# Kernel optimization log

Hardware: AMD Instinct MI355X
Metric: run time of the kernel (lower is better)

Reference implementation:

```python
import jax, jax.numpy as jnp
import numpy as np

VOCAB = 96
HIDDEN = 128
DEPTH = 500          # total ReLU iterations per character (num_layers=1)
BPTT_DEPTH = 20      # only affects backward (truncated BPTT)
EPS = 1e-6


def _rms_norm(x, scale):
    # x: (B, H). RMSNorm: x / sqrt(mean(x^2) + eps) * scale
    rms = jnp.sqrt(jnp.mean(x * x, axis=-1, keepdims=True) + EPS)
    return x / rms * scale


def setup_inputs() -> dict:
    key = jax.random.key(0)
    ks = jax.random.split(key, 6)
    B, S = 64, 32
    chars = jax.random.randint(ks[0], (B, S), 0, VOCAB)
    hidden = jnp.zeros((B, HIDDEN), dtype=jnp.float32)
    # embedding ~ N(0, 0.02)
    embed_w = 0.02 * jax.random.normal(ks[1], (VOCAB, HIDDEN), dtype=jnp.float32)
    # orthogonal recurrent weight, scaled by 1/sqrt(num_layers)=1 (num_layers=1)
    W = jnp.linalg.qr(jax.random.normal(ks[2], (HIDDEN, HIDDEN), dtype=jnp.float32))[0]
    b = jnp.zeros((HIDDEN,), dtype=jnp.float32)
    pre_scale = jnp.ones((HIDDEN,), dtype=jnp.float32)
    post_scale = jnp.ones((HIDDEN,), dtype=jnp.float32)
    # readout: xavier-uniform (VOCAB, HIDDEN), zero bias
    limit = float(np.sqrt(6.0 / (VOCAB + HIDDEN)))
    readout_w = jax.random.uniform(ks[3], (VOCAB, HIDDEN), dtype=jnp.float32,
                                   minval=-limit, maxval=limit)
    readout_b = jnp.zeros((VOCAB,), dtype=jnp.float32)
    return {"chars": chars, "hidden": hidden, "embed_w": embed_w, "W": W,
            "b": b, "pre_scale": pre_scale, "post_scale": post_scale,
            "readout_w": readout_w, "readout_b": readout_b}


def reference(chars, hidden, embed_w, W, b, pre_scale, post_scale,
              readout_w, readout_b):
    # chars: (B, S) int; hidden: (B, H)
    embeds = embed_w[chars]                       # (B, S, H)

    def recur_step(h, _):
        # h = h + relu(RMSNorm(h) @ W + e + b), e closed over per timestep
        return h, None

    def time_step(h, e):
        # DEPTH sequential residual-ReLU iterations with embed injection
        def step(hc, _):
            hc = hc + jax.nn.relu(_rms_norm(hc, pre_scale) @ W + e + b)
            return hc, None
        h, _ = jax.lax.scan(step, h, None, length=DEPTH)
        h = _rms_norm(h, post_scale)              # hidden is replaced by post_norm
        logits = h @ readout_w.T + readout_b      # (B, V)
        return h, logits

    h_final, logits = jax.lax.scan(time_step, hidden,
                                   jnp.swapaxes(embeds, 0, 1))  # scan over S
    logits = jnp.swapaxes(logits, 0, 1)           # (B, S, V)
    return logits, jax.lax.stop_gradient(h_final)
```

## Files before the change

kernel.cpp:

```cpp
#include <hip/hip_runtime.h>

#define BSZ 64
#define SLEN 32
#define HID 128
#define VOC 96
#define DEPTH 500
#define TPB 512
#define EPSV 1e-6f
#define PAD 20

typedef __attribute__((ext_vector_type(2))) float f32x2;

#if defined(__has_builtin)
#if __has_builtin(__builtin_elementwise_fma)
#define VFMA(a, b, c) __builtin_elementwise_fma((a), (b), (c))
#endif
#endif
#ifndef VFMA
__device__ __forceinline__ f32x2 vfma_(f32x2 a, f32x2 b, f32x2 c) {
    f32x2 r; r.x = fmaf(a.x, b.x, c.x); r.y = fmaf(a.y, b.y, c.y); return r;
}
#define VFMA(a, b, c) vfma_((a), (b), (c))
#endif

__device__ __forceinline__ float rsq_fast(float x) {
    float r; asm("v_rsq_f32 %0, %1" : "=v"(r) : "v"(x)); return r;
}

template <int CTRL>
__device__ __forceinline__ float qperm(float v) {
    return __int_as_float(__builtin_amdgcn_update_dpp(
        0, __float_as_int(v), CTRL, 0xF, 0xF, true));
}
#define BFLY8(v)                                                               \
    v += qperm<0xB1>(v);                                             \
    v += qperm<0x4E>(v);                                             \
    v += qperm<0x141>(v);

__global__ __launch_bounds__(TPB, 1) void rnn_char_lm(
    const int* __restrict__ chars, const float* __restrict__ hidden,
    const float* __restrict__ embed_w, const float* __restrict__ W_g,
    const float* __restrict__ b_g, const float* __restrict__ pre_s,
    const float* __restrict__ post_s, const float* __restrict__ rw_g,
    const float* __restrict__ rb_g, float* __restrict__ out)
{
    __shared__ __align__(16) float hbuf[2][8 * PAD];
    __shared__ float rwT[HID * VOC];

    const int b = blockIdx.x;
    const int tid = threadIdx.x;
    const int w = tid >> 6;
    const int lane = tid & 63;
    const int g = lane >> 3;
    const int ch = lane & 7;

    const int col0 = 16 * w + 2 * g;
    const int widx = PAD * w + 2 * g;
    const int rbase = PAD * ch;

    for (int e = tid; e < VOC * HID; e += TPB) {
        int v = e >> 7;
        int k = e & (HID - 1);
        rwT[k * VOC + v] = rw_g[e];
    }

    f32x2 W2[2][8];
#pragma unroll
    for (int q = 0; q < 8; ++q) {
        int k0 = 16 * ch + 2 * q;
        float p0 = pre_s[k0], p1 = pre_s[k0 + 1];
#pragma unroll
        for (int c = 0; c < 2; ++c) {
            f32x2 t;
            t.x = p0 * W_g[k0 * HID + col0 + c];
            t.y = p1 * W_g[(k0 + 1) * HID + col0 + c];
            W2[c][q] = t;
        }
    }
    const float2 bv  = *(const float2*)&b_g[col0];
    const float2 psv = *(const float2*)&post_s[col0];
    const float rbv = (tid < VOC) ? rb_g[tid] : 0.0f;

    float2 hc = *(const float2*)&hidden[b * HID + col0];

    if (ch == 0) *(float2*)&hbuf[0][widx] = hc;
    __syncthreads();

#define ITER(P)                                                                \
    {                                                                          \
        const float4* rb = (const float4*)&hbuf[P][rbase];                     \
        float4 x0 = rb[0], x1 = rb[1], x2 = rb[2], x3 = rb[3];                 \
        f32x2 a0 = {0,0}, a1 = {0,0}, s = {0,0};                               \
        _Pragma("unroll")                                                      \
        for (int q = 0; q < 8; ++q) {                                          \
            const float4 xq = (q < 2) ? x0 : (q < 4) ? x1 : (q < 6) ? x2 : x3; \
            f32x2 hv;                                                          \
            hv.x = (q & 1) ? xq.z : xq.x;                                      \
            hv.y = (q & 1) ? xq.w : xq.y;                                      \
            s  = VFMA(hv, hv, s);                                              \
            a0 = VFMA(hv, W2[0][q], a0);                                       \
            a1 = VFMA(hv, W2[1][q], a1);                                       \
        }                                                                      \
        float y0 = a0.x + a0.y, y1 = a1.x + a1.y;                              \
        float ssl = s.x + s.y;                                                 \
        BFLY8(y0) BFLY8(y1) BFLY8(ssl)                                         \
        const float rn = rsq_fast(fmaf(ssl, 1.0f / HID, EPSV));                \
        hc.x += fmaxf(fmaf(y0, rn, ev.x), 0.0f);                               \
        hc.y += fmaxf(fmaf(y1, rn, ev.y), 0.0f);                               \
        if (ch == 0) *(float2*)&hbuf[P ^ 1][widx] = hc;                        \
        __syncthreads();                                                       \
    }

    for (int t = 0; t < SLEN; ++t) {
        const int c = chars[b * SLEN + t];
        const float2 er = *(const float2*)&embed_w[c * HID + col0];
        float2 ev;
        ev.x = er.x + bv.x; ev.y = er.y + bv.y;

        for (int it = 0; it < DEPTH / 2; ++it) {
            ITER(0)
            ITER(1)
        }

        {
            const float4* rb = (const float4*)&hbuf[0][rbase];
            float4 x0 = rb[0], x1 = rb[1], x2 = rb[2], x3 = rb[3];
            f32x2 s = {0, 0};
            f32x2 hv;
            hv.x = x0.x; hv.y = x0.y; s = VFMA(hv, hv, s);
            hv.x = x0.z; hv.y = x0.w; s = VFMA(hv, hv, s);
            hv.x = x1.x; hv.y = x1.y; s = VFMA(hv, hv, s);
            hv.x = x1.z; hv.y = x1.w; s = VFMA(hv, hv, s);
            hv.x = x2.x; hv.y = x2.y; s = VFMA(hv, hv, s);
            hv.x = x2.z; hv.y = x2.w; s = VFMA(hv, hv, s);
            hv.x = x3.x; hv.y = x3.y; s = VFMA(hv, hv, s);
            hv.x = x3.z; hv.y = x3.w; s = VFMA(hv, hv, s);
            float ssl = s.x + s.y;
            BFLY8(ssl)
            const float rnp = 1.0f / sqrtf(ssl * (1.0f / HID) + EPSV);
            hc.x *= rnp * psv.x;
            hc.y *= rnp * psv.y;
            __syncthreads();
            if (ch == 0) *(float2*)&hbuf[0][widx] = hc;
            __syncthreads();
        }

        if (tid < VOC) {
            float acc0 = 0.0f, acc1 = 0.0f;
#pragma unroll
            for (int C = 0; C < 8; ++C) {
#pragma unroll
                for (int m4 = 0; m4 < 4; ++m4) {
                    const float4 x = *(const float4*)&hbuf[0][PAD * C + 4 * m4];
                    const int k = 16 * C + 4 * m4;
                    acc0 = fmaf(x.x, rwT[(k + 0) * VOC + tid], acc0);
                    acc1 = fmaf(x.y, rwT[(k + 1) * VOC + tid], acc1);
                    acc0 = fmaf(x.z, rwT[(k + 2) * VOC + tid], acc0);
                    acc1 = fmaf(x.w, rwT[(k + 3) * VOC + tid], acc1);
                }
            }
            out[(b * SLEN + t) * VOC + tid] = acc0 + acc1 + rbv;
        }
    }

    if (ch == 0)
        *(float2*)&out[BSZ * SLEN * VOC + b * HID + col0] = hc;

#undef ITER
}

extern "C" void kernel_launch(void* const* d_in, const int* in_sizes, int n_in,
                              void* d_out, int out_size, void* d_ws, size_t ws_size,
                              hipStream_t stream)
{
    const int* chars      = (const int*)d_in[0];
    const float* hidden   = (const float*)d_in[1];
    const float* embed_w  = (const float*)d_in[2];
    const float* W_g      = (const float*)d_in[3];
    const float* b_g      = (const float*)d_in[4];
    const float* pre_s    = (const float*)d_in[5];
    const float* post_s   = (const float*)d_in[6];
    const float* rw_g     = (const float*)d_in[7];
    const float* rb_g     = (const float*)d_in[8];
    float* out            = (float*)d_out;

    rnn_char_lm<<<dim3(BSZ), dim3(TPB), 0, stream>>>(
        chars, hidden, embed_w, W_g, b_g, pre_s, post_s, rw_g, rb_g, out);
}
```

Measured before the change: 4.344 ms.

## Repartition recurrence over 256 threads with 8 columns and 16-way K split

Halves the block to 256 threads (4 waves). Each thread now computes 8 output columns over an 8-element K slice, and partial sums are reduced across 16 lanes with a 4-step DPP butterfly. This is meant to cut the per-iteration barrier cost by syncing fewer waves and to read less LDS per thread. In exchange each thread does more FMAs and DPP reductions per step, which lengthens the serial critical path of each of the 500 dependent iterations.

```diff
diff --git a/kernel.cpp b/kernel.cpp
--- a/kernel.cpp
+++ b/kernel.cpp
@@ -5,9 +5,9 @@
 #define HID 128
 #define VOC 96
 #define DEPTH 500
-#define TPB 512
+#define TPB 256
 #define EPSV 1e-6f
-#define PAD 20
+#define CHK 12
 
 typedef __attribute__((ext_vector_type(2))) float f32x2;
 
@@ -32,10 +32,11 @@
     return __int_as_float(__builtin_amdgcn_update_dpp(
         0, __float_as_int(v), CTRL, 0xF, 0xF, true));
 }
-#define BFLY8(v)                                                               \
-    v += qperm<0xB1>(v);                                             \
-    v += qperm<0x4E>(v);                                             \
-    v += qperm<0x141>(v);
+#define BFLY16(v)                                                              \
+    v += qperm<0xB1>(v);                                                       \
+    v += qperm<0x4E>(v);                                                       \
+    v += qperm<0x141>(v);                                                      \
+    v += qperm<0x140>(v);
 
 __global__ __launch_bounds__(TPB, 1) void rnn_char_lm(
     const int* __restrict__ chars, const float* __restrict__ hidden,
@@ -44,19 +45,20 @@
     const float* __restrict__ post_s, const float* __restrict__ rw_g,
     const float* __restrict__ rb_g, float* __restrict__ out)
 {
-    __shared__ __align__(16) float hbuf[2][8 * PAD];
+    __shared__ __align__(16) float hbuf[2][16 * CHK];
     __shared__ float rwT[HID * VOC];
 
     const int b = blockIdx.x;
     const int tid = threadIdx.x;
     const int w = tid >> 6;
     const int lane = tid & 63;
-    const int g = lane >> 3;
-    const int ch = lane & 7;
-
-    const int col0 = 16 * w + 2 * g;
-    const int widx = PAD * w + 2 * g;
-    const int rbase = PAD * ch;
+    const int g = lane >> 4;
+    const int ch = lane & 15;
+
+    const int col0 = 32 * w + 8 * g;
+    const int cblk = 4 * w + g;
+    const int rbase = CHK * ch;
+    const int wslot = CHK * cblk + 4 * (ch & 1);
 
     for (int e = tid; e < VOC * HID; e += TPB) {
         int v = e >> 7;
@@ -64,58 +66,102 @@
         rwT[k * VOC + v] = rw_g[e];
     }
 
-    f32x2 W2[2][8];
-#pragma unroll
-    for (int q = 0; q < 8; ++q) {
-        int k0 = 16 * ch + 2 * q;
+    f32x2 W2[8][4];
+#pragma unroll
+    for (int q = 0; q < 4; ++q) {
+        int k0 = 8 * ch + 2 * q;
         float p0 = pre_s[k0], p1 = pre_s[k0 + 1];
 #pragma unroll
-        for (int c = 0; c < 2; ++c) {
+        for (int c = 0; c < 8; ++c) {
             f32x2 t;
             t.x = p0 * W_g[k0 * HID + col0 + c];
             t.y = p1 * W_g[(k0 + 1) * HID + col0 + c];
             W2[c][q] = t;
         }
     }
-    const float2 bv  = *(const float2*)&b_g[col0];
-    const float2 psv = *(const float2*)&post_s[col0];
+    float bvv[8], psvv[8];
+    {
+        float4 b0 = *(const float4*)&b_g[col0];
+        float4 b1 = *(const float4*)&b_g[col0 + 4];
+        float4 p0 = *(const float4*)&post_s[col0];
+        float4 p1 = *(const float4*)&post_s[col0 + 4];
+        bvv[0]=b0.x; bvv[1]=b0.y; bvv[2]=b0.z; bvv[3]=b0.w;
+        bvv[4]=b1.x; bvv[5]=b1.y; bvv[6]=b1.z; bvv[7]=b1.w;
+        psvv[0]=p0.x; psvv[1]=p0.y; psvv[2]=p0.z; psvv[3]=p0.w;
+        psvv[4]=p1.x; psvv[5]=p1.y; psvv[6]=p1.z; psvv[7]=p1.w;
+    }
     const float rbv = (tid < VOC) ? rb_g[tid] : 0.0f;
 
-    float2 hc = *(const float2*)&hidden[b * HID + col0];
-
-    if (ch == 0) *(float2*)&hbuf[0][widx] = hc;
+    float hc[8];
+    {
+        float4 h0 = *(const float4*)&hidden[b * HID + col0];
+        float4 h1 = *(const float4*)&hidden[b * HID + col0 + 4];
+        hc[0]=h0.x; hc[1]=h0.y; hc[2]=h0.z; hc[3]=h0.w;
+        hc[4]=h1.x; hc[5]=h1.y; hc[6]=h1.z; hc[7]=h1.w;
+    }
+    if (ch == 0) {
+        *(float4*)&hbuf[0][CHK * cblk]     = make_float4(hc[0],hc[1],hc[2],hc[3]);
+        *(float4*)&hbuf[0][CHK * cblk + 4] = make_float4(hc[4],hc[5],hc[6],hc[7]);
+    }
     __syncthreads();
 
 #define ITER(P)                                                                \
     {                                                                          \
         const float4* rb = (const float4*)&hbuf[P][rbase];                     \
-        float4 x0 = rb[0], x1 = rb[1], x2 = rb[2], x3 = rb[3];                 \
-        f32x2 a0 = {0,0}, a1 = {0,0}, s = {0,0};                               \
+        float4 x0 = rb[0], x1 = rb[1];                                         \
+        f32x2 a0={0,0},a1={0,0},a2={0,0},a3={0,0};                             \
+        f32x2 a4={0,0},a5={0,0},a6={0,0},a7={0,0},s={0,0};                     \
         _Pragma("unroll")                                                      \
-        for (int q = 0; q < 8; ++q) {                                          \
-            const float4 xq = (q < 2) ? x0 : (q < 4) ? x1 : (q < 6) ? x2 : x3; \
+        for (int q = 0; q < 4; ++q) {                                          \
             f32x2 hv;                                                          \
-            hv.x = (q & 1) ? xq.z : xq.x;                                      \
-            hv.y = (q & 1) ? xq.w : xq.y;                                      \
+            hv.x = (q == 0) ? x0.x : (q == 1) ? x0.z : (q == 2) ? x1.x : x1.z; \
+            hv.y = (q == 0) ? x0.y : (q == 1) ? x0.w : (q == 2) ? x1.y : x1.w; \
             s  = VFMA(hv, hv, s);                                              \
             a0 = VFMA(hv, W2[0][q], a0);                                       \
             a1 = VFMA(hv, W2[1][q], a1);                                       \
+            a2 = VFMA(hv, W2[2][q], a2);                                       \
+            a3 = VFMA(hv, W2[3][q], a3);                                       \
+            a4 = VFMA(hv, W2[4][q], a4);                                       \
+            a5 = VFMA(hv, W2[5][q], a5);                                       \
+            a6 = VFMA(hv, W2[6][q], a6);                                       \
+            a7 = VFMA(hv, W2[7][q], a7);                                       \
         }                                                                      \
-        float y0 = a0.x + a0.y, y1 = a1.x + a1.y;                              \
+        float y0=a0.x+a0.y, y1=a1.x+a1.y, y2=a2.x+a2.y, y3=a3.x+a3.y;          \
+        float y4=a4.x+a4.y, y5=a5.x+a5.y, y6=a6.x+a6.y, y7=a7.x+a7.y;          \
         float ssl = s.x + s.y;                                                 \
-        BFLY8(y0) BFLY8(y1) BFLY8(ssl)                                         \
+        BFLY16(y0) BFLY16(y1) BFLY16(y2) BFLY16(y3)                            \
+        BFLY16(y4) BFLY16(y5) BFLY16(y6) BFLY16(y7) BFLY16(ssl)                \
         const float rn = rsq_fast(fmaf(ssl, 1.0f / HID, EPSV));                \
-        hc.x += fmaxf(fmaf(y0, rn, ev.x), 0.0f);                               \
-        hc.y += fmaxf(fmaf(y1, rn, ev.y), 0.0f);                               \
-        if (ch == 0) *(float2*)&hbuf[P ^ 1][widx] = hc;                        \
+        hc[0] += fmaxf(fmaf(y0, rn, evv[0]), 0.0f);                            \
+        hc[1] += fmaxf(fmaf(y1, rn, evv[1]), 0.0f);                            \
+        hc[2] += fmaxf(fmaf(y2, rn, evv[2]), 0.0f);                            \
+        hc[3] += fmaxf(fmaf(y3, rn, evv[3]), 0.0f);                            \
+        hc[4] += fmaxf(fmaf(y4, rn, evv[4]), 0.0f);                            \
+        hc[5] += fmaxf(fmaf(y5, rn, evv[5]), 0.0f);                            \
+        hc[6] += fmaxf(fmaf(y6, rn, evv[6]), 0.0f);                            \
+        hc[7] += fmaxf(fmaf(y7, rn, evv[7]), 0.0f);                            \
+        if (ch < 2) {                                                          \
+            float4 wd;                                                         \
+            wd.x = ch ? hc[4] : hc[0];                                         \
+            wd.y = ch ? hc[5] : hc[1];                                         \
+            wd.z = ch ? hc[6] : hc[2];                                         \
+            wd.w = ch ? hc[7] : hc[3];                                         \
+            *(float4*)&hbuf[P ^ 1][wslot] = wd;                                \
+        }                                                                      \
         __syncthreads();                                                       \
     }
 
     for (int t = 0; t < SLEN; ++t) {
         const int c = chars[b * SLEN + t];
-        const float2 er = *(const float2*)&embed_w[c * HID + col0];
-        float2 ev;
-        ev.x = er.x + bv.x; ev.y = er.y + bv.y;
+        float evv[8];
+        {
+            float4 e0 = *(const float4*)&embed_w[c * HID + col0];
+            float4 e1 = *(const float4*)&embed_w[c * HID + col0 + 4];
+            evv[0]=e0.x+bvv[0]; evv[1]=e0.y+bvv[1];
+            evv[2]=e0.z+bvv[2]; evv[3]=e0.w+bvv[3];
+            evv[4]=e1.x+bvv[4]; evv[5]=e1.y+bvv[5];
+            evv[6]=e1.z+bvv[6]; evv[7]=e1.w+bvv[7];
+        }
 
         for (int it = 0; it < DEPTH / 2; ++it) {
             ITER(0)
@@ -124,47 +170,52 @@
 
         {
             const float4* rb = (const float4*)&hbuf[0][rbase];
-            float4 x0 = rb[0], x1 = rb[1], x2 = rb[2], x3 = rb[3];
+            float4 x0 = rb[0], x1 = rb[1];
             f32x2 s = {0, 0};
             f32x2 hv;
             hv.x = x0.x; hv.y = x0.y; s = VFMA(hv, hv, s);
             hv.x = x0.z; hv.y = x0.w; s = VFMA(hv, hv, s);
             hv.x = x1.x; hv.y = x1.y; s = VFMA(hv, hv, s);
             hv.x = x1.z; hv.y = x1.w; s = VFMA(hv, hv, s);
-            hv.x = x2.x; hv.y = x2.y; s = VFMA(hv, hv, s);
-            hv.x = x2.z; hv.y = x2.w; s = VFMA(hv, hv, s);
-            hv.x = x3.x; hv.y = x3.y; s = VFMA(hv, hv, s);
-            hv.x = x3.z; hv.y = x3.w; s = VFMA(hv, hv, s);
             float ssl = s.x + s.y;
-            BFLY8(ssl)
+            BFLY16(ssl)
             const float rnp = 1.0f / sqrtf(ssl * (1.0f / HID) + EPSV);
-            hc.x *= rnp * psv.x;
-            hc.y *= rnp * psv.y;
+#pragma unroll
+            for (int cc = 0; cc < 8; ++cc) hc[cc] *= rnp * psvv[cc];
             __syncthreads();
-            if (ch == 0) *(float2*)&hbuf[0][widx] = hc;
+            if (ch == 0) {
+                *(float4*)&hbuf[0][CHK * cblk]     = make_float4(hc[0],hc[1],hc[2],hc[3]);
+                *(float4*)&hbuf[0][CHK * cblk + 4] = make_float4(hc[4],hc[5],hc[6],hc[7]);
+            }
             __syncthreads();
         }
 
         if (tid < VOC) {
             float acc0 = 0.0f, acc1 = 0.0f;
 #pragma unroll
-            for (int C = 0; C < 8; ++C) {
-#pragma unroll
-                for (int m4 = 0; m4 < 4; ++m4) {
-                    const float4 x = *(const float4*)&hbuf[0][PAD * C + 4 * m4];
-                    const int k = 16 * C + 4 * m4;
-                    acc0 = fmaf(x.x, rwT[(k + 0) * VOC + tid], acc0);
-                    acc1 = fmaf(x.y, rwT[(k + 1) * VOC + tid], acc1);
-                    acc0 = fmaf(x.z, rwT[(k + 2) * VOC + tid], acc0);
-                    acc1 = fmaf(x.w, rwT[(k + 3) * VOC + tid], acc1);
-                }
+            for (int C = 0; C < 16; ++C) {
+                const float4 x0 = *(const float4*)&hbuf[0][CHK * C];
+                const float4 x1 = *(const float4*)&hbuf[0][CHK * C + 4];
+                const int k = 8 * C;
+                acc0 = fmaf(x0.x, rwT[(k + 0) * VOC + tid], acc0);
+                acc1 = fmaf(x0.y, rwT[(k + 1) * VOC + tid], acc1);
+                acc0 = fmaf(x0.z, rwT[(k + 2) * VOC + tid], acc0);
+                acc1 = fmaf(x0.w, rwT[(k + 3) * VOC + tid], acc1);
+                acc0 = fmaf(x1.x, rwT[(k + 4) * VOC + tid], acc0);
+                acc1 = fmaf(x1.y, rwT[(k + 5) * VOC + tid], acc1);
+                acc0 = fmaf(x1.z, rwT[(k + 6) * VOC + tid], acc0);
+                acc1 = fmaf(x1.w, rwT[(k + 7) * VOC + tid], acc1);
             }
             out[(b * SLEN + t) * VOC + tid] = acc0 + acc1 + rbv;
         }
     }
 
-    if (ch == 0)
-        *(float2*)&out[BSZ * SLEN * VOC + b * HID + col0] = hc;
+    if (ch == 0) {
+        *(float4*)&out[BSZ * SLEN * VOC + b * HID + col0] =
+            make_float4(hc[0], hc[1], hc[2], hc[3]);
+        *(float4*)&out[BSZ * SLEN * VOC + b * HID + col0 + 4] =
+            make_float4(hc[4], hc[5], hc[6], hc[7]);
+    }
 
 #undef ITER
 }
```

Result: slower. 5.043 ms (+16.1%).
